# Kernel optimization log

Measured on AMD Instinct MI355X. Metric: run time of the kernel, lower is better.

The kernel has to match this reference:

```python
import jax, jax.numpy as jnp
import numpy as np
from jax import lax

C = 512
BN_EPS = 1e-5
GLN_EPS = 1e-8


def setup_inputs() -> dict:
    key = jax.random.key(0)
    ks = jax.random.split(key, 10)
    B, T = 16, 4000
    x = jax.random.normal(ks[0], (B, C, T), dtype=jnp.float32)
    # BatchNorm1d params (eval mode: affine + running stats)
    bn_gamma = jax.random.normal(ks[1], (C,), dtype=jnp.float32) * 0.1 + 1.0
    bn_beta = jax.random.normal(ks[2], (C,), dtype=jnp.float32) * 0.1
    bn_mean = jax.random.normal(ks[3], (C,), dtype=jnp.float32) * 0.1
    bn_var = jax.random.uniform(ks[4], (C,), dtype=jnp.float32) + 0.5
    # depthwise Conv1d(512,512,3,groups=512,bias=False): kernel [O=C, I=1, K=3]
    dw_w = jax.random.normal(ks[5], (C, 1, 3), dtype=jnp.float32) * (1.0 / np.sqrt(3.0))
    # PReLU default: single shared parameter init 0.25
    prelu_a = jnp.full((1,), 0.25, dtype=jnp.float32)
    # GlobalLayerNorm(512) affine params
    gln_gamma = jnp.ones((C,), dtype=jnp.float32)
    gln_beta = jnp.zeros((C,), dtype=jnp.float32)
    # pointwise Conv1d(512,512,1,bias=False): weight [O, I]
    pw_w = jax.random.normal(ks[6], (C, C), dtype=jnp.float32) * (1.0 / np.sqrt(C))
    return {"x": x, "bn_gamma": bn_gamma, "bn_beta": bn_beta, "bn_mean": bn_mean,
            "bn_var": bn_var, "dw_w": dw_w, "prelu_a": prelu_a,
            "gln_gamma": gln_gamma, "gln_beta": gln_beta, "pw_w": pw_w}


def reference(x, bn_gamma, bn_beta, bn_mean, bn_var, dw_w, prelu_a,
              gln_gamma, gln_beta, pw_w):
    # ReLU
    h = jax.nn.relu(x)
    # BatchNorm1d (eval mode, running stats), per-channel affine over [B,C,T]
    scale = (bn_gamma * lax.rsqrt(bn_var + BN_EPS))[None, :, None]
    h = h * scale + (bn_beta - bn_mean * bn_gamma * lax.rsqrt(bn_var + BN_EPS))[None, :, None]
    # depthwise conv1d, kernel 3, pad 1, groups=C
    h = lax.conv_general_dilated(h, dw_w, window_strides=(1,), padding=((1, 1),),
                                 feature_group_count=C,
                                 dimension_numbers=("NCH", "OIH", "NCH"))
    # PReLU (single shared slope)
    h = jnp.where(h >= 0, h, prelu_a[0] * h)
    # GlobalLayerNorm: normalize over (C, T) per sample, per-channel affine
    mean = jnp.mean(h, axis=(1, 2), keepdims=True)
    var = jnp.mean(jnp.square(h - mean), axis=(1, 2), keepdims=True)
    h = gln_gamma[None, :, None] * (h - mean) * lax.rsqrt(var + GLN_EPS) + gln_beta[None, :, None]
    # pointwise 1x1 conv == channel GEMM
    h = jnp.einsum("oc,bct->bot", pw_w, h)
    # residual
    return h + x
```

## Files before the change

kernel.cpp:

```cpp
#include <hip/hip_runtime.h>
#include <stdint.h>

#define B_ 16
#define C_ 512
#define T_ 4000
#define TPAD 4096

typedef float f32x4 __attribute__((ext_vector_type(4)));
typedef __bf16 bf16x8 __attribute__((ext_vector_type(8)));

__device__ inline unsigned short f2b(float f) {
  uint32_t u = __builtin_bit_cast(uint32_t, f);
  u = (u + 0x7fffu + ((u >> 16) & 1u)) >> 16;
  return (unsigned short)u;
}
__device__ inline float b2f(unsigned short h) {
  uint32_t u = ((uint32_t)h) << 16;
  return __builtin_bit_cast(float, u);
}
__device__ inline void gl_lds16(const void* g, void* s) {
  __builtin_amdgcn_global_load_lds(
      (const __attribute__((address_space(1))) uint32_t*)g,
      (__attribute__((address_space(3))) uint32_t*)s, 16, 0, 0);
}


__global__ void k_init(float* wsf) {
  int i = threadIdx.x;
  if (i < 32) wsf[i] = 0.f;
}

__global__ __launch_bounds__(64) void k_prepw(const float* __restrict__ pw,
                                              const float* __restrict__ gamma,
                                              const float* __restrict__ beta,
                                              unsigned short* __restrict__ Wp,
                                              float* __restrict__ wsf) {
  int o = blockIdx.x, l = threadIdx.x;
  float a1 = 0.f, a2 = 0.f;
  for (int j = 0; j < 8; ++j) {
    int c = j * 64 + l;
    float wv = pw[o * 512 + c];
    unsigned short wb = f2b(wv * gamma[c]);
    Wp[o * 512 + c] = wb;
    a1 += b2f(wb);
    a2 += wv * beta[c];
  }
  for (int s = 32; s > 0; s >>= 1) { a1 += __shfl_down(a1, s); a2 += __shfl_down(a2, s); }
  if (l == 0) { wsf[64 + o] = a1; wsf[576 + o] = a2; }
}

__global__ __launch_bounds__(512) void k_front(const float* __restrict__ x,
    const float* __restrict__ bng, const float* __restrict__ bnb,
    const float* __restrict__ bnm, const float* __restrict__ bnv,
    const float* __restrict__ dw, const float* __restrict__ pa,
    unsigned short* __restrict__ hT, float* __restrict__ wsf) {
  __shared__ unsigned short hs[256 * 64] __attribute__((aligned(16)));
  __shared__ float psc[64], pbi[64], pq0[64], pq1[64], pq2[64];
  __shared__ float partial[16];
  int tid = threadIdx.x;
  int l = tid & 63, w = tid >> 6;
  int tb = blockIdx.x;
  int cb = blockIdx.y;
  int b  = blockIdx.z;
  int t0 = tb * 256;
  if (tid < 64) {
    int c = cb * 64 + tid;
    float sc = bng[c] * rsqrtf(bnv[c] + 1e-5f);
    psc[tid] = sc;
    pbi[tid] = bnb[c] - bnm[c] * sc;
    pq0[tid] = dw[3 * c];
    pq1[tid] = dw[3 * c + 1];
    pq2[tid] = dw[3 * c + 2];
  }
  float alpha = pa[0];
  __syncthreads();

  int t = t0 + 4 * l;
  bool full = (t + 3 < T_);
  bool has_l = (t0 > 0);
  bool has_r = (t0 + 256 < T_);
  float sum = 0.f, sq = 0.f;
  int cs_x = (l & 7) << 3;

#pragma unroll 2
  for (int i = 0; i < 8; ++i) {
    int cl = w * 8 + i;
    const float* xr = x + ((size_t)b * C_ + cb * 64 + cl) * T_;
    float sc = psc[cl], bi = pbi[cl];
    float w0 = pq0[cl], w1 = pq1[cl], w2 = pq2[cl];
    f32x4 u;
    if (full) {
      const f32x4 v = *(const f32x4*)(xr + t);
      u.x = fmaxf(v.x, 0.f) * sc + bi;
      u.y = fmaxf(v.y, 0.f) * sc + bi;
      u.z = fmaxf(v.z, 0.f) * sc + bi;
      u.w = fmaxf(v.w, 0.f) * sc + bi;
    } else {
      u = (f32x4){0.f, 0.f, 0.f, 0.f};
    }
    float el = has_l ? (fmaxf(xr[t0 - 1], 0.f) * sc + bi) : 0.f;
    float er = has_r ? (fmaxf(xr[t0 + 256], 0.f) * sc + bi) : 0.f;
    float up = __shfl_up(u.w, 1);   if (l == 0)  up = el;
    float un = __shfl_down(u.x, 1); if (l == 63) un = er;
    float h[4];
    h[0] = w0 * up  + w1 * u.x + w2 * u.y;
    h[1] = w0 * u.x + w1 * u.y + w2 * u.z;
    h[2] = w0 * u.y + w1 * u.z + w2 * u.w;
    h[3] = w0 * u.z + w1 * u.w + w2 * un;
    int cs = cl ^ cs_x;
#pragma unroll
    for (int j = 0; j < 4; ++j) {
      float p = h[j] >= 0.f ? h[j] : alpha * h[j];
      if (!full) p = 0.f;
      sum += p; sq += p * p;
      hs[(4 * l + j) * 64 + cs] = f2b(p);
    }
  }

  for (int s = 32; s > 0; s >>= 1) { sum += __shfl_down(sum, s); sq += __shfl_down(sq, s); }
  if (l == 0) { partial[w] = sum; partial[8 + w] = sq; }
  __syncthreads();
  if (tid == 0) {
    float a = 0.f, c2 = 0.f;
    for (int k = 0; k < 8; ++k) { a += partial[k]; c2 += partial[8 + k]; }
    atomicAdd(&wsf[b], a);
    atomicAdd(&wsf[16 + b], c2);
  }

  unsigned short* dstb = hT + ((size_t)b * TPAD + t0) * 512 + cb * 64;
#pragma unroll
  for (int p = 0; p < 4; ++p) {
    int idx = p * 512 + tid;
    int tl = idx >> 3, g = idx & 7;
    int gs = g ^ ((tl >> 2) & 7);
    uint4 val = *(const uint4*)(hs + tl * 64 + gs * 8);
    *(uint4*)(dstb + (size_t)tl * 512 + g * 8) = val;
  }
}

__global__ void k_finalize(float* wsf) {
  int b = threadIdx.x;
  if (b < 16) {
    float n = (float)C_ * (float)T_;
    float mean = wsf[b] / n;
    float var = wsf[16 + b] / n - mean * mean;
    wsf[32 + b] = mean;
    wsf[48 + b] = rsqrtf(fmaxf(var, 0.f) + 1e-8f);
  }
}

__global__ __launch_bounds__(512, 2) void k_gemm(const unsigned short* __restrict__ Wp,
    const unsigned short* __restrict__ hT, const float* __restrict__ x,
    const float* __restrict__ wsf, float* __restrict__ out) {
  __shared__ unsigned short As0[8192], As1[8192], Bs0[8192], Bs1[8192];
  int tid = threadIdx.x;
  int l = tid & 63, w = tid >> 6;
  int nb = blockIdx.x, mb = blockIdx.y, b = blockIdx.z;
  int wm = w >> 2, wn = w & 3;
  const unsigned short* hTb = hT + (size_t)b * TPAD * 512;

  int aoff[2], boff[2], ldso[2];
#pragma unroll
  for (int r = 0; r < 2; ++r) {
    int i = r * 512 + tid;
    int row = i >> 2, s = i & 3;
    int ksl = (s ^ ((row >> 1) & 3)) << 3;
    aoff[r] = (mb * 256 + row) * 512 + ksl;
    boff[r] = (nb * 256 + row) * 512 + ksl;
    ldso[r] = i * 8;
  }

  int aro[8], bro[4];
#pragma unroll
  for (int fm = 0; fm < 8; ++fm) {
    int row = wm * 128 + fm * 16 + (l & 15);
    int slot = (l >> 4) ^ ((row >> 1) & 3);
    aro[fm] = row * 32 + slot * 8;
  }
#pragma unroll
  for (int fn = 0; fn < 4; ++fn) {
    int row = wn * 64 + fn * 16 + (l & 15);
    int slot = (l >> 4) ^ ((row >> 1) & 3);
    bro[fn] = row * 32 + slot * 8;
  }

#pragma unroll
  for (int r = 0; r < 2; ++r) {
    gl_lds16(Wp + aoff[r], As0 + ldso[r]);
    gl_lds16(hTb + boff[r], Bs0 + ldso[r]);
  }
#pragma unroll
  for (int r = 0; r < 2; ++r) {
    gl_lds16(Wp + aoff[r] + 32, As1 + ldso[r]);
    gl_lds16(hTb + boff[r] + 32, Bs1 + ldso[r]);
  }

  unsigned short *cA = As0, *cB = Bs0;
  unsigned short *oA = As1, *oB = Bs1;

  f32x4 acc[8][4] = {};
#pragma unroll 1
  for (int kt = 0; kt < 16; ++kt) {
    if (kt == 15) asm volatile("s_waitcnt vmcnt(0)" ::: "memory");
    else          asm volatile("s_waitcnt vmcnt(4)" ::: "memory");
    __builtin_amdgcn_s_barrier();
    __builtin_amdgcn_sched_barrier(0);
    bf16x8 af[8], bv[4];
#pragma unroll
    for (int fm = 0; fm < 8; ++fm) af[fm] = *(const bf16x8*)(cA + aro[fm]);
#pragma unroll
    for (int fn = 0; fn < 4; ++fn) bv[fn] = *(const bf16x8*)(cB + bro[fn]);
    asm volatile("s_waitcnt lgkmcnt(0)" ::: "memory");
    __builtin_amdgcn_s_barrier();
    __builtin_amdgcn_sched_barrier(0);
    if (kt < 14) {
      int kofs = (kt + 2) * 32;
#pragma unroll
      for (int r = 0; r < 2; ++r) {
        gl_lds16(Wp + aoff[r] + kofs, cA + ldso[r]);
        gl_lds16(hTb + boff[r] + kofs, cB + ldso[r]);
      }
    }
    __builtin_amdgcn_s_setprio(1);
#pragma unroll
    for (int fm = 0; fm < 8; ++fm)
#pragma unroll
      for (int fn = 0; fn < 4; ++fn)
        acc[fm][fn] = __builtin_amdgcn_mfma_f32_16x16x32_bf16(af[fm], bv[fn], acc[fm][fn], 0, 0, 0);
    __builtin_amdgcn_s_setprio(0);
    unsigned short* t1 = cA; cA = oA; oA = t1;
    unsigned short* t2 = cB; cB = oB; oB = t2;
  }

  float mean = wsf[32 + b], rstd = wsf[48 + b];
  float mr = mean * rstd;
#pragma unroll
  for (int fm = 0; fm < 8; ++fm) {
    int o0 = mb * 256 + wm * 128 + fm * 16 + ((l >> 4) << 2);
    float bias[4];
#pragma unroll
    for (int j = 0; j < 4; ++j) {
      int o = o0 + j;
      bias[j] = wsf[576 + o] - mr * wsf[64 + o];
    }
#pragma unroll
    for (int fn = 0; fn < 4; ++fn) {
      int t = nb * 256 + wn * 64 + fn * 16 + (l & 15);
      if (t < T_) {
#pragma unroll
        for (int j = 0; j < 4; ++j) {
          int o = o0 + j;
          size_t idx = ((size_t)b * C_ + o) * T_ + t;
          out[idx] = rstd * acc[fm][fn][j] + bias[j] + x[idx];
        }
      }
    }
  }
}

extern "C" void kernel_launch(void* const* d_in, const int* in_sizes, int n_in,
                              void* d_out, int out_size, void* d_ws, size_t ws_size,
                              hipStream_t stream) {
  const float* x   = (const float*)d_in[0];
  const float* bng = (const float*)d_in[1];
  const float* bnb = (const float*)d_in[2];
  const float* bnm = (const float*)d_in[3];
  const float* bnv = (const float*)d_in[4];
  const float* dw  = (const float*)d_in[5];
  const float* pa  = (const float*)d_in[6];
  const float* gg  = (const float*)d_in[7];
  const float* gb  = (const float*)d_in[8];
  const float* pw  = (const float*)d_in[9];
  float* out = (float*)d_out;
  float* wsf = (float*)d_ws;
  unsigned short* Wp = (unsigned short*)((char*)d_ws + 8192);
  unsigned short* hT = (unsigned short*)((char*)d_ws + (1 << 20));

  k_init<<<dim3(1), dim3(64), 0, stream>>>(wsf);
  k_prepw<<<dim3(512), dim3(64), 0, stream>>>(pw, gg, gb, Wp, wsf);
  k_front<<<dim3(16, 8, 16), dim3(512), 0, stream>>>(x, bng, bnb, bnm, bnv, dw, pa, hT, wsf);
  k_finalize<<<dim3(1), dim3(64), 0, stream>>>(wsf);
  k_gemm<<<dim3(16, 2, 16), dim3(512), 0, stream>>>(Wp, hT, x, wsf, out);
}
```

Measured before the change: 153.5 us.

## Drop init/finalize kernels and batch front-end x loads up front

Zeroing of the stat accumulators moves into k_prepw and the mean/rstd finalization moves into the GEMM epilogue, which removes two tiny kernel launches and their serialization gaps. In k_front, all eight channel rows of x are loaded into registers before compute, so more global loads are in flight at once. The cost is higher register pressure in k_front and redundant per-block stat computation in the GEMM.

Measured after the change: 153.0 us. Within noise of the previous version (-0.3%).

```diff
diff --git a/kernel.cpp b/kernel.cpp
--- a/kernel.cpp
+++ b/kernel.cpp
@@ -24,11 +24,6 @@
       (__attribute__((address_space(3))) uint32_t*)s, 16, 0, 0);
 }
 
-
-__global__ void k_init(float* wsf) {
-  int i = threadIdx.x;
-  if (i < 32) wsf[i] = 0.f;
-}
 
 __global__ __launch_bounds__(64) void k_prepw(const float* __restrict__ pw,
                                               const float* __restrict__ gamma,
@@ -36,6 +31,7 @@
                                               unsigned short* __restrict__ Wp,
                                               float* __restrict__ wsf) {
   int o = blockIdx.x, l = threadIdx.x;
+  if (o == 0 && l < 32) wsf[l] = 0.f;
   float a1 = 0.f, a2 = 0.f;
   for (int j = 0; j < 8; ++j) {
     int c = j * 64 + l;
@@ -79,27 +75,36 @@
   bool full = (t + 3 < T_);
   bool has_l = (t0 > 0);
   bool has_r = (t0 + 256 < T_);
+
+  f32x4 xv[8];
+  float xel[8], xer[8];
+#pragma unroll
+  for (int i = 0; i < 8; ++i) {
+    const float* xr = x + ((size_t)b * C_ + cb * 64 + w * 8 + i) * T_;
+    if (full) xv[i] = *(const f32x4*)(xr + t);
+    else      xv[i] = (f32x4){0.f, 0.f, 0.f, 0.f};
+    xel[i] = has_l ? xr[t0 - 1] : 0.f;
+    xer[i] = has_r ? xr[t0 + 256] : 0.f;
+  }
+
   float sum = 0.f, sq = 0.f;
   int cs_x = (l & 7) << 3;
-
-#pragma unroll 2
+#pragma unroll
   for (int i = 0; i < 8; ++i) {
     int cl = w * 8 + i;
-    const float* xr = x + ((size_t)b * C_ + cb * 64 + cl) * T_;
     float sc = psc[cl], bi = pbi[cl];
     float w0 = pq0[cl], w1 = pq1[cl], w2 = pq2[cl];
     f32x4 u;
     if (full) {
-      const f32x4 v = *(const f32x4*)(xr + t);
-      u.x = fmaxf(v.x, 0.f) * sc + bi;
-      u.y = fmaxf(v.y, 0.f) * sc + bi;
-      u.z = fmaxf(v.z, 0.f) * sc + bi;
-      u.w = fmaxf(v.w, 0.f) * sc + bi;
+      u.x = fmaxf(xv[i].x, 0.f) * sc + bi;
+      u.y = fmaxf(xv[i].y, 0.f) * sc + bi;
+      u.z = fmaxf(xv[i].z, 0.f) * sc + bi;
+      u.w = fmaxf(xv[i].w, 0.f) * sc + bi;
     } else {
       u = (f32x4){0.f, 0.f, 0.f, 0.f};
     }
-    float el = has_l ? (fmaxf(xr[t0 - 1], 0.f) * sc + bi) : 0.f;
-    float er = has_r ? (fmaxf(xr[t0 + 256], 0.f) * sc + bi) : 0.f;
+    float el = has_l ? (fmaxf(xel[i], 0.f) * sc + bi) : 0.f;
+    float er = has_r ? (fmaxf(xer[i], 0.f) * sc + bi) : 0.f;
     float up = __shfl_up(u.w, 1);   if (l == 0)  up = el;
     float un = __shfl_down(u.x, 1); if (l == 63) un = er;
     float h[4];
@@ -135,17 +140,6 @@
     int gs = g ^ ((tl >> 2) & 7);
     uint4 val = *(const uint4*)(hs + tl * 64 + gs * 8);
     *(uint4*)(dstb + (size_t)tl * 512 + g * 8) = val;
-  }
-}
-
-__global__ void k_finalize(float* wsf) {
-  int b = threadIdx.x;
-  if (b < 16) {
-    float n = (float)C_ * (float)T_;
-    float mean = wsf[b] / n;
-    float var = wsf[16 + b] / n - mean * mean;
-    wsf[32 + b] = mean;
-    wsf[48 + b] = rsqrtf(fmaxf(var, 0.f) + 1e-8f);
   }
 }
 
@@ -232,7 +226,10 @@
     unsigned short* t2 = cB; cB = oB; oB = t2;
   }
 
-  float mean = wsf[32 + b], rstd = wsf[48 + b];
+  float n = (float)C_ * (float)T_;
+  float mean = wsf[b] / n;
+  float var = wsf[16 + b] / n - mean * mean;
+  float rstd = rsqrtf(fmaxf(var, 0.f) + 1e-8f);
   float mr = mean * rstd;
 #pragma unroll
   for (int fm = 0; fm < 8; ++fm) {
@@ -276,9 +273,7 @@
   unsigned short* Wp = (unsigned short*)((char*)d_ws + 8192);
   unsigned short* hT = (unsigned short*)((char*)d_ws + (1 << 20));
 
-  k_init<<<dim3(1), dim3(64), 0, stream>>>(wsf);
   k_prepw<<<dim3(512), dim3(64), 0, stream>>>(pw, gg, gb, Wp, wsf);
   k_front<<<dim3(16, 8, 16), dim3(512), 0, stream>>>(x, bng, bnb, bnm, bnv, dw, pa, hT, wsf);
-  k_finalize<<<dim3(1), dim3(64), 0, stream>>>(wsf);
   k_gemm<<<dim3(16, 2, 16), dim3(512), 0, stream>>>(Wp, hT, x, wsf, out);
 }
```
